# Kernel tuning notes

Measured on AMD Instinct MI355X. Metric: run time of the kernel, lower is better.

Reference implementation:

```python
import jax, jax.numpy as jnp
import numpy as np

NUM_HEADS = 16

def setup_inputs() -> dict:
    key = jax.random.key(0)
    k_x, k_wq, k_bq, k_wo, k_bo = jax.random.split(key, 5)
    B, S, D = 4, 2048, 1024
    x = jax.random.normal(k_x, (B, S, D), dtype=jnp.float32)
    # Flax Dense default init: lecun_normal for kernel, zeros for bias; use small normals here.
    w_qkv = jax.random.normal(k_wq, (D, 3 * D), dtype=jnp.float32) * (D ** -0.5)
    b_qkv = jnp.zeros((3 * D,), dtype=jnp.float32)
    w_out = jax.random.normal(k_wo, (D, D), dtype=jnp.float32) * (D ** -0.5)
    b_out = jnp.zeros((D,), dtype=jnp.float32)
    return {"x": x, "w_qkv": w_qkv, "b_qkv": b_qkv, "w_out": w_out, "b_out": b_out}

def reference(x, w_qkv, b_qkv, w_out, b_out):
    B, S, D = x.shape
    H = NUM_HEADS
    hd = D // H
    scale = hd ** -0.5
    qkv = x @ w_qkv + b_qkv                                  # [B,S,3D]
    qkv = qkv.reshape(B, S, 3, H, hd)
    qkv = jnp.transpose(qkv, (2, 0, 3, 1, 4))                # [3,B,H,S,hd]
    q, k, v = qkv[0], qkv[1], qkv[2]
    attn = jnp.einsum("bhqd,bhkd->bhqk", q, k) * scale       # [B,H,S,S]
    attn = jax.nn.softmax(attn, axis=-1)
    out = jnp.einsum("bhqk,bhkd->bhqd", attn, v)             # [B,H,S,hd]
    out = jnp.transpose(out, (0, 2, 1, 3)).reshape(B, S, D)
    return out @ w_out + b_out
```

## Files before the change

kernel.cpp:

```cpp
#include <hip/hip_runtime.h>
#include <cstdint>
#include <cstddef>

#define B_    4
#define S_    2048
#define D_    1024
#define H_    16
#define HD_   64
#define M_    8192
#define NQKV  3072

typedef __bf16 bf16;
typedef __bf16 bf16x4 __attribute__((ext_vector_type(4)));
typedef __bf16 bf16x8 __attribute__((ext_vector_type(8)));
typedef float  f32x2  __attribute__((ext_vector_type(2)));
typedef float  f32x4  __attribute__((ext_vector_type(4)));
typedef float  f32x16 __attribute__((ext_vector_type(16)));
typedef unsigned short u16x4 __attribute__((ext_vector_type(4)));
typedef uint32_t u32x2 __attribute__((ext_vector_type(2)));
typedef uint32_t u32x4 __attribute__((ext_vector_type(4)));

__device__ __forceinline__ void gl2lds16(const void* g, void* l) {
  __builtin_amdgcn_global_load_lds(
      (__attribute__((address_space(1))) void*)(uintptr_t)g,
      (__attribute__((address_space(3))) void*)l, 16, 0, 0);
}

__device__ __forceinline__ uint32_t pkbf16(float a, float b) {
  union { bf16 h[2]; uint32_t u; } z;
  z.h[0] = (bf16)a; z.h[1] = (bf16)b;
  return z.u;
}

__global__ __launch_bounds__(256) void cast_f32_bf16(const float* __restrict__ in,
                                                     bf16* __restrict__ out, int n4) {
  int i = blockIdx.x * 256 + threadIdx.x;
  if (i >= n4) return;
  float4 v = ((const float4*)in)[i];
  bf16x4 o;
  o[0] = (bf16)v.x; o[1] = (bf16)v.y; o[2] = (bf16)v.z; o[3] = (bf16)v.w;
  ((bf16x4*)out)[i] = o;
}

__global__ __launch_bounds__(256) void transpose_cast(const float* __restrict__ in,
                                                      bf16* __restrict__ out, int R, int C) {
  __shared__ float tile[32][33];
  int bx = blockIdx.x * 32, by = blockIdx.y * 32;
  int tx = threadIdx.x, ty = threadIdx.y;
#pragma unroll
  for (int i = 0; i < 32; i += 8)
    tile[ty + i][tx] = in[(size_t)(by + ty + i) * C + bx + tx];
  __syncthreads();
#pragma unroll
  for (int i = 0; i < 32; i += 8)
    out[(size_t)(bx + ty + i) * R + by + tx] = (bf16)tile[tx][ty + i];
}

template <bool OUT_BF16>
__global__ __launch_bounds__(256) void gemm_bt(const bf16* __restrict__ A,
                                               const bf16* __restrict__ Bt,
                                               const float* __restrict__ bias,
                                               void* __restrict__ Cptr,
                                               int M, int N, int K) {
  __shared__ __align__(16) bf16 As[128 * 64];
  __shared__ __align__(16) bf16 Bs[128 * 64];
  const int tid  = threadIdx.x;
  const int lane = tid & 63, w = tid >> 6;
  const int lo   = lane & 15, quad = lane >> 4;
  const int xcd = blockIdx.x & 7, g = blockIdx.x >> 3;
  const int mi  = g & 7,          n = g >> 3;
  const int bm  = (xcd * 8 + mi) * 128, bn = n * 128;
  const int wm = (w >> 1) * 64,    wn = (w & 1) * 64;

  f32x4 acc[4][4];
  const f32x4 zero = {0.f, 0.f, 0.f, 0.f};
#pragma unroll
  for (int i = 0; i < 4; ++i)
#pragma unroll
    for (int j = 0; j < 4; ++j) acc[i][j] = zero;

  for (int k0 = 0; k0 < K; k0 += 64) {
#pragma unroll
    for (int c = 0; c < 4; ++c) {
      int seg = c * 4 + w;
      int idx = seg * 512 + lane * 8;
      int row = idx >> 6, col = idx & 63;
      gl2lds16(A  + (size_t)(bm + row) * K + k0 + col, As + seg * 512);
      gl2lds16(Bt + (size_t)(bn + row) * K + k0 + col, Bs + seg * 512);
    }
    __syncthreads();
#pragma unroll
    for (int ks = 0; ks < 2; ++ks) {
      bf16x8 av[4], bv[4];
#pragma unroll
      for (int i = 0; i < 4; ++i)
        av[i] = *(const bf16x8*)&As[(wm + i * 16 + lo) * 64 + ks * 32 + quad * 8];
#pragma unroll
      for (int j = 0; j < 4; ++j)
        bv[j] = *(const bf16x8*)&Bs[(wn + j * 16 + lo) * 64 + ks * 32 + quad * 8];
#pragma unroll
      for (int i = 0; i < 4; ++i)
#pragma unroll
        for (int j = 0; j < 4; ++j)
          acc[i][j] = __builtin_amdgcn_mfma_f32_16x16x32_bf16(av[i], bv[j], acc[i][j], 0, 0, 0);
    }
    __syncthreads();
  }
#pragma unroll
  for (int j = 0; j < 4; ++j) {
    int cg = bn + wn + j * 16 + lo;
    float bsv = bias[cg];
#pragma unroll
    for (int i = 0; i < 4; ++i) {
      int rg = bm + wm + i * 16 + quad * 4;
#pragma unroll
      for (int r = 0; r < 4; ++r) {
        float v = acc[i][j][r] + bsv;
        if (OUT_BF16) ((bf16*)Cptr)[(size_t)(rg + r) * N + cg] = (bf16)v;
        else          ((float*)Cptr)[(size_t)(rg + r) * N + cg] = v;
      }
    }
  }
}

__global__ __launch_bounds__(256, 2) void gemm_bt_wide(const bf16* __restrict__ A,
                                                       const bf16* __restrict__ Bt,
                                                       const float* __restrict__ bias,
                                                       bf16* __restrict__ Cptr,
                                                       int M, int N, int K) {
  __shared__ __align__(16) bf16 As[128 * 64];
  __shared__ __align__(16) bf16 Bs[256 * 64];
  const int tid  = threadIdx.x;
  const int lane = tid & 63, w = tid >> 6;
  const int lo   = lane & 15, quad = lane >> 4;
  const int xcd = blockIdx.x & 7, g = blockIdx.x >> 3;
  const int mi  = g & 7,          n = g >> 3;
  const int bm  = (xcd * 8 + mi) * 128, bn = n * 256;
  const int wm = (w >> 1) * 64,    wn = (w & 1) * 128;

  f32x4 acc[4][8];
  const f32x4 zero = {0.f, 0.f, 0.f, 0.f};
#pragma unroll
  for (int i = 0; i < 4; ++i)
#pragma unroll
    for (int j = 0; j < 8; ++j) acc[i][j] = zero;

  for (int k0 = 0; k0 < K; k0 += 64) {
#pragma unroll
    for (int c = 0; c < 4; ++c) {
      int seg = c * 4 + w;
      int idx = seg * 512 + lane * 8;
      int row = idx >> 6, col = idx & 63;
      gl2lds16(A + (size_t)(bm + row) * K + k0 + col, As + seg * 512);
    }
#pragma unroll
    for (int c = 0; c < 8; ++c) {
      int seg = c * 4 + w;
      int idx = seg * 512 + lane * 8;
      int row = idx >> 6, col = idx & 63;
      gl2lds16(Bt + (size_t)(bn + row) * K + k0 + col, Bs + seg * 512);
    }
    __syncthreads();
#pragma unroll
    for (int ks = 0; ks < 2; ++ks) {
      bf16x8 av[4], bv[8];
#pragma unroll
      for (int i = 0; i < 4; ++i)
        av[i] = *(const bf16x8*)&As[(wm + i * 16 + lo) * 64 + ks * 32 + quad * 8];
#pragma unroll
      for (int j = 0; j < 8; ++j)
        bv[j] = *(const bf16x8*)&Bs[(wn + j * 16 + lo) * 64 + ks * 32 + quad * 8];
#pragma unroll
      for (int i = 0; i < 4; ++i)
#pragma unroll
        for (int j = 0; j < 8; ++j)
          acc[i][j] = __builtin_amdgcn_mfma_f32_16x16x32_bf16(av[i], bv[j], acc[i][j], 0, 0, 0);
    }
    __syncthreads();
  }
#pragma unroll
  for (int j = 0; j < 8; ++j) {
    int cg = bn + wn + j * 16 + lo;
    float bsv = bias[cg];
#pragma unroll
    for (int i = 0; i < 4; ++i) {
      int rg = bm + wm + i * 16 + quad * 4;
#pragma unroll
      for (int r = 0; r < 4; ++r)
        Cptr[(size_t)(rg + r) * N + cg] = (bf16)(acc[i][j][r] + bsv);
    }
  }
}

__global__ __launch_bounds__(256, 2) void flash_attn(const bf16* __restrict__ qkv,
                                                     bf16* __restrict__ out) {
  __shared__ __align__(16) bf16 smem[16384];
  bf16* const Ksm = smem;
  bf16* const Vsm = smem + 8192;

  const int tid  = threadIdx.x;
  const int lane = tid & 63, wq = tid >> 6;
  const int l31  = lane & 31;
  const int e    = lane >> 5;
  const int hi8  = e * 8, hi4 = e * 4;

  const int bid = blockIdx.x;
  const int qb  = bid >> 6;
  const int bh  = bid & 63;
  const int h   = bh & 15;
  const int b   = bh >> 4;
  const int q0  = qb * 256;
  const size_t rowb = (size_t)b * S_;
  const bf16* qbase = qkv + rowb * NQKV + h * HD_;
  const bf16* kbase = qbase + D_;
  const bf16* vbase = qbase + 2 * D_;

  bf16x8 qfA[4], qfB[4];
  {
    const bf16* qrow0 = qbase + (size_t)(q0 + wq * 64 + l31) * NQKV;
    const bf16* qrow1 = qrow0 + (size_t)32 * NQKV;
#pragma unroll
    for (int c = 0; c < 4; ++c) {
      qfA[c] = *(const bf16x8*)(qrow0 + c * 16 + hi8);
      qfB[c] = *(const bf16x8*)(qrow1 + c * 16 + hi8);
    }
  }

  int kq_off[2];
#pragma unroll
  for (int it = 0; it < 2; ++it) {
    int ci = it * 256 + tid;
    int s  = ci >> 3;
    int x  = (ci & 7) ^ (s & 7);
    kq_off[it] = s * NQKV + x * 8;
  }
  int vs_d[2], vs_s[2], vs_off[2];
#pragma unroll
  for (int u = 0; u < 2; ++u) {
    int idx = u * 256 + tid;
    int d0 = (idx & 31) * 2;
    int s0 = (idx >> 5) * 4;
    vs_d[u] = d0;
    vs_s[u] = s0;
    vs_off[u] = (((s0 >> 3) ^ ((d0 >> 1) & 7)) * 8) + (s0 & 7);
  }

  uint32_t vreg[2][4];

#pragma unroll
  for (int it = 0; it < 2; ++it)
    gl2lds16(kbase + kq_off[it], Ksm + (it * 256 + wq * 64) * 8);
#pragma unroll
  for (int u = 0; u < 2; ++u)
#pragma unroll
    for (int j = 0; j < 4; ++j)
      vreg[u][j] = *(const uint32_t*)(vbase + (size_t)(vs_s[u] + j) * NQKV + vs_d[u]);

  const f32x16 zero16 = {0.f,0.f,0.f,0.f,0.f,0.f,0.f,0.f,0.f,0.f,0.f,0.f,0.f,0.f,0.f,0.f};
  f32x16 oacc[2][2];
  oacc[0][0] = zero16; oacc[0][1] = zero16;
  oacc[1][0] = zero16; oacc[1][1] = zero16;
  f32x2 psA = {0.f, 0.f}, psB = {0.f, 0.f};
  const float c2 = 0.125f * 1.44269504088896341f;

  for (int kt = 0; kt < 32; ++kt) {
    const int buf = kt & 1;
#pragma unroll
    for (int u = 0; u < 2; ++u) {
      int d0 = vs_d[u];
      uint32_t lo0 = __builtin_amdgcn_perm(vreg[u][1], vreg[u][0], 0x05040100u);
      uint32_t lo1 = __builtin_amdgcn_perm(vreg[u][3], vreg[u][2], 0x05040100u);
      uint32_t hi0 = __builtin_amdgcn_perm(vreg[u][1], vreg[u][0], 0x07060302u);
      uint32_t hi1 = __builtin_amdgcn_perm(vreg[u][3], vreg[u][2], 0x07060302u);
      u32x2 lov = {lo0, lo1}, hiv = {hi0, hi1};
      *(u32x2*)&Vsm[buf * 4096 + (d0 + 0) * 64 + vs_off[u]] = lov;
      *(u32x2*)&Vsm[buf * 4096 + (d0 + 1) * 64 + vs_off[u]] = hiv;
    }
    __syncthreads();

    {
      int ktn = (kt + 1 < 32) ? kt + 1 : 31;
      const bf16* kb = kbase + (size_t)ktn * 64 * NQKV;
#pragma unroll
      for (int it = 0; it < 2; ++it)
        gl2lds16(kb + kq_off[it], Ksm + (buf ^ 1) * 4096 + (it * 256 + wq * 64) * 8);
    }
    {
      int ktn = (kt + 1 < 32) ? kt + 1 : 31;
      const bf16* vb = vbase + (size_t)ktn * 64 * NQKV;
#pragma unroll
      for (int u = 0; u < 2; ++u)
#pragma unroll
        for (int j = 0; j < 4; ++j)
          vreg[u][j] = *(const uint32_t*)(vb + (size_t)(vs_s[u] + j) * NQKV + vs_d[u]);
    }

#pragma unroll
    for (int kk = 0; kk < 2; ++kk) {
      f32x16 sA = zero16, sB = zero16;
      int srow = kk * 32 + l31;
      int swz  = (srow & 7) * 8;
#pragma unroll
      for (int c = 0; c < 4; ++c) {
        bf16x8 kf = *(const bf16x8*)&Ksm[buf * 4096 + srow * 64 + ((c * 16 + hi8) ^ swz)];
        sA = __builtin_amdgcn_mfma_f32_32x32x16_bf16(kf, qfA[c], sA, 0, 0, 0);
        sB = __builtin_amdgcn_mfma_f32_32x32x16_bf16(kf, qfB[c], sB, 0, 0, 0);
      }

      uint32_t Q8a[8], Q8b[8];
#pragma unroll
      for (int i = 0; i < 8; ++i) {
        f32x2 sva, svb;
        sva[0] = sA[2 * i]; sva[1] = sA[2 * i + 1];
        svb[0] = sB[2 * i]; svb[1] = sB[2 * i + 1];
        f32x2 ta = sva * c2 - 16.0f;
        f32x2 tb = svb * c2 - 16.0f;
        float a0 = __builtin_amdgcn_exp2f(ta[0]);
        float a1 = __builtin_amdgcn_exp2f(ta[1]);
        float b0 = __builtin_amdgcn_exp2f(tb[0]);
        float b1 = __builtin_amdgcn_exp2f(tb[1]);
        psA += (f32x2){a0, a1};
        psB += (f32x2){b0, b1};
        Q8a[i] = pkbf16(a0, a1);
        Q8b[i] = pkbf16(b0, b1);
      }

#pragma unroll
      for (int mh = 0; mh < 2; ++mh) {
        const int m = kk * 2 + mh, bq = mh * 4;
        u32x4 pda, pdb;
#if __has_builtin(__builtin_amdgcn_permlane32_swap)
        u32x2 wa0 = __builtin_amdgcn_permlane32_swap(Q8a[bq],     Q8a[bq + 2], false, false);
        u32x2 wa1 = __builtin_amdgcn_permlane32_swap(Q8a[bq + 1], Q8a[bq + 3], false, false);
        pda[0] = wa0[0]; pda[1] = wa1[0]; pda[2] = wa0[1]; pda[3] = wa1[1];
        u32x2 wb0 = __builtin_amdgcn_permlane32_swap(Q8b[bq],     Q8b[bq + 2], false, false);
        u32x2 wb1 = __builtin_amdgcn_permlane32_swap(Q8b[bq + 1], Q8b[bq + 3], false, false);
        pdb[0] = wb0[0]; pdb[1] = wb1[0]; pdb[2] = wb0[1]; pdb[3] = wb1[1];
#else
        {
          uint32_t s0 = e ? Q8a[bq]     : Q8a[bq + 2];
          uint32_t s1 = e ? Q8a[bq + 1] : Q8a[bq + 3];
          uint32_t r0 = __shfl_xor(s0, 32);
          uint32_t r1 = __shfl_xor(s1, 32);
          pda[0] = e ? r0 : Q8a[bq];
          pda[1] = e ? r1 : Q8a[bq + 1];
          pda[2] = e ? Q8a[bq + 2] : r0;
          pda[3] = e ? Q8a[bq + 3] : r1;
        }
        {
          uint32_t s0 = e ? Q8b[bq]     : Q8b[bq + 2];
          uint32_t s1 = e ? Q8b[bq + 1] : Q8b[bq + 3];
          uint32_t r0 = __shfl_xor(s0, 32);
          uint32_t r1 = __shfl_xor(s1, 32);
          pdb[0] = e ? r0 : Q8b[bq];
          pdb[1] = e ? r1 : Q8b[bq + 1];
          pdb[2] = e ? Q8b[bq + 2] : r0;
          pdb[3] = e ? Q8b[bq + 3] : r1;
        }
#endif
        bf16x8 pfa = __builtin_bit_cast(bf16x8, pda);
        bf16x8 pfb = __builtin_bit_cast(bf16x8, pdb);
#pragma unroll
        for (int dt = 0; dt < 2; ++dt) {
          int drow = dt * 32 + l31;
          int swv  = (drow >> 1) & 7;
          bf16x8 vf = *(const bf16x8*)&Vsm[buf * 4096 + drow * 64 + (((m * 2 + e) ^ swv) * 8)];
          oacc[dt][0] = __builtin_amdgcn_mfma_f32_32x32x16_bf16(vf, pfa, oacc[dt][0], 0, 0, 0);
          oacc[dt][1] = __builtin_amdgcn_mfma_f32_32x32x16_bf16(vf, pfb, oacc[dt][1], 0, 0, 0);
        }
      }
    }
  }

  float lsumA = psA[0] + psA[1];
  float lsumB = psB[0] + psB[1];
  lsumA += __shfl_xor(lsumA, 32);
  lsumB += __shfl_xor(lsumB, 32);

  __syncthreads();
  bf16* Os = smem;
  {
    float invA = 1.f / lsumA;
    float invB = 1.f / lsumB;
#pragma unroll
    for (int qs = 0; qs < 2; ++qs) {
      float inv = qs ? invB : invA;
      int ql = wq * 64 + qs * 32 + l31;
      int swO = (ql >> 1) & 7;
#pragma unroll
      for (int dt = 0; dt < 2; ++dt) {
#pragma unroll
        for (int g = 0; g < 4; ++g) {
          bf16x4 ov;
#pragma unroll
          for (int jj = 0; jj < 4; ++jj)
            ov[jj] = (bf16)(oacc[dt][qs][g * 4 + jj] * inv);
          *(bf16x4*)&Os[ql * 64 + (((dt * 4 + g) ^ swO) * 8) + hi4] = ov;
        }
      }
    }
  }
  __syncthreads();
#pragma unroll
  for (int it = 0; it < 8; ++it) {
    int idx = it * 256 + tid;
    int row = idx >> 3, c8 = idx & 7;
    bf16x8 t = *(const bf16x8*)&Os[row * 64 + ((c8 ^ ((row >> 1) & 7)) * 8)];
    *(bf16x8*)&out[(rowb + q0 + row) * D_ + h * HD_ + c8 * 8] = t;
  }
}

extern "C" void kernel_launch(void* const* d_in, const int* in_sizes, int n_in,
                              void* d_out, int out_size, void* d_ws, size_t ws_size,
                              hipStream_t stream) {
  const float* x     = (const float*)d_in[0];
  const float* w_qkv = (const float*)d_in[1];
  const float* b_qkv = (const float*)d_in[2];
  const float* w_out = (const float*)d_in[3];
  const float* b_out = (const float*)d_in[4];
  float* out = (float*)d_out;

  char* ws = (char*)d_ws;
  bf16* xb    = (bf16*)(ws);
  bf16* wqkvT = (bf16*)(ws + (size_t)16777216);
  bf16* woutT = (bf16*)(ws + (size_t)23068672);
  bf16* qkvb  = (bf16*)(ws + (size_t)25165824);
  bf16* attnb = (bf16*)(ws + (size_t)75497472);

  cast_f32_bf16<<<(M_ * D_ / 4 + 255) / 256, 256, 0, stream>>>(x, xb, M_ * D_ / 4);
  transpose_cast<<<dim3(NQKV / 32, D_ / 32), dim3(32, 8), 0, stream>>>(w_qkv, wqkvT, D_, NQKV);
  transpose_cast<<<dim3(D_ / 32, D_ / 32), dim3(32, 8), 0, stream>>>(w_out, woutT, D_, D_);

  gemm_bt_wide<<<(M_ / 128) * (NQKV / 256), 256, 0, stream>>>(
      xb, wqkvT, b_qkv, qkvb, M_, NQKV, D_);

  flash_attn<<<B_ * H_ * (S_ / 256), 256, 0, stream>>>(qkvb, attnb);

  gemm_bt<false><<<(M_ / 128) * (D_ / 128), 256, 0, stream>>>(
      attnb, woutT, b_out, (void*)out, M_, D_, D_);
}
```

Measured before the change: 283.2 us.

## Deepen K/V prefetch pipeline and raise wave priority around MFMA blocks

The attention loop is restructured so that the K tile's async global-to-LDS copy for the next step and the V register loads two steps ahead are issued before compute. The V transpose-write into the other LDS buffer moves after compute, and each step ends with one explicit waitcnt plus barrier. This removes the mid-iteration barrier and hides global-load latency behind the MFMA work. s_setprio is also raised around the MFMA groups so waves doing matrix work get issue priority. The cost is a second set of V staging registers, which adds register pressure, and a hand-written vmcnt that depends on the exact order in which loads are issued.

```diff
diff --git a/kernel.cpp b/kernel.cpp
--- a/kernel.cpp
+++ b/kernel.cpp
@@ -245,16 +245,7 @@
     vs_off[u] = (((s0 >> 3) ^ ((d0 >> 1) & 7)) * 8) + (s0 & 7);
   }
 
-  uint32_t vreg[2][4];
-
-#pragma unroll
-  for (int it = 0; it < 2; ++it)
-    gl2lds16(kbase + kq_off[it], Ksm + (it * 256 + wq * 64) * 8);
-#pragma unroll
-  for (int u = 0; u < 2; ++u)
-#pragma unroll
-    for (int j = 0; j < 4; ++j)
-      vreg[u][j] = *(const uint32_t*)(vbase + (size_t)(vs_s[u] + j) * NQKV + vs_d[u]);
+  uint32_t vE[2][4], vO[2][4];
 
   const f32x16 zero16 = {0.f,0.f,0.f,0.f,0.f,0.f,0.f,0.f,0.f,0.f,0.f,0.f,0.f,0.f,0.f,0.f};
   f32x16 oacc[2][2];
@@ -263,49 +254,48 @@
   f32x2 psA = {0.f, 0.f}, psB = {0.f, 0.f};
   const float c2 = 0.125f * 1.44269504088896341f;
 
-  for (int kt = 0; kt < 32; ++kt) {
-    const int buf = kt & 1;
-#pragma unroll
-    for (int u = 0; u < 2; ++u) {
-      int d0 = vs_d[u];
-      uint32_t lo0 = __builtin_amdgcn_perm(vreg[u][1], vreg[u][0], 0x05040100u);
-      uint32_t lo1 = __builtin_amdgcn_perm(vreg[u][3], vreg[u][2], 0x05040100u);
-      uint32_t hi0 = __builtin_amdgcn_perm(vreg[u][1], vreg[u][0], 0x07060302u);
-      uint32_t hi1 = __builtin_amdgcn_perm(vreg[u][3], vreg[u][2], 0x07060302u);
-      u32x2 lov = {lo0, lo1}, hiv = {hi0, hi1};
-      *(u32x2*)&Vsm[buf * 4096 + (d0 + 0) * 64 + vs_off[u]] = lov;
-      *(u32x2*)&Vsm[buf * 4096 + (d0 + 1) * 64 + vs_off[u]] = hiv;
-    }
-    __syncthreads();
-
-    {
-      int ktn = (kt + 1 < 32) ? kt + 1 : 31;
-      const bf16* kb = kbase + (size_t)ktn * 64 * NQKV;
-#pragma unroll
-      for (int it = 0; it < 2; ++it)
-        gl2lds16(kb + kq_off[it], Ksm + (buf ^ 1) * 4096 + (it * 256 + wq * 64) * 8);
-    }
-    {
-      int ktn = (kt + 1 < 32) ? kt + 1 : 31;
-      const bf16* vb = vbase + (size_t)ktn * 64 * NQKV;
-#pragma unroll
-      for (int u = 0; u < 2; ++u)
-#pragma unroll
-        for (int j = 0; j < 4; ++j)
-          vreg[u][j] = *(const uint32_t*)(vb + (size_t)(vs_s[u] + j) * NQKV + vs_d[u]);
-    }
-
+#define KDMA(KT, PB) {                                                      \
+    const bf16* kb_ = kbase + (size_t)(KT) * 64 * NQKV;                     \
+    _Pragma("unroll")                                                       \
+    for (int it = 0; it < 2; ++it)                                          \
+      gl2lds16(kb_ + kq_off[it], Ksm + (PB) * 4096 + (it * 256 + wq * 64) * 8); \
+  }
+#define VLOAD(KT, VR) {                                                     \
+    const bf16* vb_ = vbase + (size_t)(KT) * 64 * NQKV;                     \
+    _Pragma("unroll")                                                       \
+    for (int u = 0; u < 2; ++u)                                             \
+      _Pragma("unroll")                                                     \
+      for (int j = 0; j < 4; ++j)                                           \
+        VR[u][j] = *(const uint32_t*)(vb_ + (size_t)(vs_s[u] + j) * NQKV + vs_d[u]); \
+  }
+#define VWRITE(VR, PB) {                                                    \
+    _Pragma("unroll")                                                       \
+    for (int u = 0; u < 2; ++u) {                                           \
+      int d0_ = vs_d[u];                                                    \
+      uint32_t lo0 = __builtin_amdgcn_perm(VR[u][1], VR[u][0], 0x05040100u);\
+      uint32_t lo1 = __builtin_amdgcn_perm(VR[u][3], VR[u][2], 0x05040100u);\
+      uint32_t hi0 = __builtin_amdgcn_perm(VR[u][1], VR[u][0], 0x07060302u);\
+      uint32_t hi1 = __builtin_amdgcn_perm(VR[u][3], VR[u][2], 0x07060302u);\
+      u32x2 lov = {lo0, lo1}, hiv = {hi0, hi1};                             \
+      *(u32x2*)&Vsm[(PB) * 4096 + (d0_ + 0) * 64 + vs_off[u]] = lov;        \
+      *(u32x2*)&Vsm[(PB) * 4096 + (d0_ + 1) * 64 + vs_off[u]] = hiv;        \
+    }                                                                       \
+  }
+
+  auto compute = [&](int P) __attribute__((always_inline)) {
 #pragma unroll
     for (int kk = 0; kk < 2; ++kk) {
       f32x16 sA = zero16, sB = zero16;
       int srow = kk * 32 + l31;
       int swz  = (srow & 7) * 8;
+      __builtin_amdgcn_s_setprio(1);
 #pragma unroll
       for (int c = 0; c < 4; ++c) {
-        bf16x8 kf = *(const bf16x8*)&Ksm[buf * 4096 + srow * 64 + ((c * 16 + hi8) ^ swz)];
+        bf16x8 kf = *(const bf16x8*)&Ksm[P * 4096 + srow * 64 + ((c * 16 + hi8) ^ swz)];
         sA = __builtin_amdgcn_mfma_f32_32x32x16_bf16(kf, qfA[c], sA, 0, 0, 0);
         sB = __builtin_amdgcn_mfma_f32_32x32x16_bf16(kf, qfB[c], sB, 0, 0, 0);
       }
+      __builtin_amdgcn_s_setprio(0);
 
       uint32_t Q8a[8], Q8b[8];
 #pragma unroll
@@ -360,17 +350,46 @@
 #endif
         bf16x8 pfa = __builtin_bit_cast(bf16x8, pda);
         bf16x8 pfb = __builtin_bit_cast(bf16x8, pdb);
+        __builtin_amdgcn_s_setprio(1);
 #pragma unroll
         for (int dt = 0; dt < 2; ++dt) {
           int drow = dt * 32 + l31;
           int swv  = (drow >> 1) & 7;
-          bf16x8 vf = *(const bf16x8*)&Vsm[buf * 4096 + drow * 64 + (((m * 2 + e) ^ swv) * 8)];
+          bf16x8 vf = *(const bf16x8*)&Vsm[P * 4096 + drow * 64 + (((m * 2 + e) ^ swv) * 8)];
           oacc[dt][0] = __builtin_amdgcn_mfma_f32_32x32x16_bf16(vf, pfa, oacc[dt][0], 0, 0, 0);
           oacc[dt][1] = __builtin_amdgcn_mfma_f32_32x32x16_bf16(vf, pfb, oacc[dt][1], 0, 0, 0);
         }
+        __builtin_amdgcn_s_setprio(0);
       }
     }
-  }
+  };
+
+#define BODY(KT, P, VWR, VLD) {                                             \
+    int kn1 = (KT) + 1 < 32 ? (KT) + 1 : 31;                                \
+    int kn2 = (KT) + 2 < 32 ? (KT) + 2 : 31;                                \
+    KDMA(kn1, (P) ^ 1);                           \
+    VLOAD(kn2, VLD);               \
+    compute(P);                                                             \
+    VWRITE(VWR, (P) ^ 1);                  \
+    asm volatile("s_waitcnt vmcnt(8) lgkmcnt(0)" ::: "memory");             \
+    __builtin_amdgcn_s_barrier();                                           \
+  }
+
+  KDMA(0, 0);
+  VLOAD(0, vE);
+  VLOAD(1, vO);
+  VWRITE(vE, 0);
+  asm volatile("s_waitcnt vmcnt(8) lgkmcnt(0)" ::: "memory");
+  __builtin_amdgcn_s_barrier();
+
+  for (int t = 0; t < 16; ++t) {
+    BODY(2 * t,     0, vO, vE);
+    BODY(2 * t + 1, 1, vE, vO);
+  }
+#undef BODY
+#undef VWRITE
+#undef VLOAD
+#undef KDMA
 
   float lsumA = psA[0] + psA[1];
   float lsumB = psB[0] + psB[1];
```

Result: no change. 286.2 us (+1.1%).

## Split flash attention KV range across two wave groups and merge partial outputs

Applied to the files above, without the earlier changes.

Doubles the attention block to 512 threads: two groups of four waves each process half of the key/value sequence for the same 256 queries, with separate LDS buffers. Partial row sums and output accumulators are combined through LDS at the end before normalising and writing. It also raises wave priority around the MFMA sections with s_setprio. This is meant to shorten each block's serial KV loop and raise waves per CU, at the cost of double the LDS per block and an extra reduction pass. Skipping the running max remains safe here because the fixed exp offset is reused unchanged.

```diff
diff --git a/kernel.cpp b/kernel.cpp
--- a/kernel.cpp
+++ b/kernel.cpp
@@ -192,17 +192,18 @@
   }
 }
 
-__global__ __launch_bounds__(256, 2) void flash_attn(const bf16* __restrict__ qkv,
+__global__ __launch_bounds__(512, 4) void flash_attn(const bf16* __restrict__ qkv,
                                                      bf16* __restrict__ out) {
-  __shared__ __align__(16) bf16 smem[16384];
-  bf16* const Ksm = smem;
-  bf16* const Vsm = smem + 8192;
+  __shared__ __align__(16) bf16 smem[32768];
 
   const int tid  = threadIdx.x;
-  const int lane = tid & 63, wq = tid >> 6;
+  const int lane = tid & 63;
+  const int wq   = (tid >> 6) & 3;
+  const int grp  = tid >> 8;
+  const int t8   = tid & 255;
   const int l31  = lane & 31;
   const int e    = lane >> 5;
-  const int hi8  = e * 8, hi4 = e * 4;
+  const int hi8  = e * 8;
 
   const int bid = blockIdx.x;
   const int qb  = bid >> 6;
@@ -212,8 +213,11 @@
   const int q0  = qb * 256;
   const size_t rowb = (size_t)b * S_;
   const bf16* qbase = qkv + rowb * NQKV + h * HD_;
-  const bf16* kbase = qbase + D_;
-  const bf16* vbase = qbase + 2 * D_;
+  const bf16* kbase = qbase + D_     + (size_t)(grp * 16) * 64 * NQKV;
+  const bf16* vbase = qbase + 2 * D_ + (size_t)(grp * 16) * 64 * NQKV;
+
+  bf16* const Ksg = smem + grp * 16384;
+  bf16* const Vsg = Ksg + 8192;
 
   bf16x8 qfA[4], qfB[4];
   {
@@ -229,7 +233,7 @@
   int kq_off[2];
 #pragma unroll
   for (int it = 0; it < 2; ++it) {
-    int ci = it * 256 + tid;
+    int ci = it * 256 + t8;
     int s  = ci >> 3;
     int x  = (ci & 7) ^ (s & 7);
     kq_off[it] = s * NQKV + x * 8;
@@ -237,7 +241,7 @@
   int vs_d[2], vs_s[2], vs_off[2];
 #pragma unroll
   for (int u = 0; u < 2; ++u) {
-    int idx = u * 256 + tid;
+    int idx = u * 256 + t8;
     int d0 = (idx & 31) * 2;
     int s0 = (idx >> 5) * 4;
     vs_d[u] = d0;
@@ -249,7 +253,7 @@
 
 #pragma unroll
   for (int it = 0; it < 2; ++it)
-    gl2lds16(kbase + kq_off[it], Ksm + (it * 256 + wq * 64) * 8);
+    gl2lds16(kbase + kq_off[it], Ksg + (it * 256 + wq * 64) * 8);
 #pragma unroll
   for (int u = 0; u < 2; ++u)
 #pragma unroll
@@ -263,7 +267,7 @@
   f32x2 psA = {0.f, 0.f}, psB = {0.f, 0.f};
   const float c2 = 0.125f * 1.44269504088896341f;
 
-  for (int kt = 0; kt < 32; ++kt) {
+  for (int kt = 0; kt < 16; ++kt) {
     const int buf = kt & 1;
 #pragma unroll
     for (int u = 0; u < 2; ++u) {
@@ -273,20 +277,20 @@
       uint32_t hi0 = __builtin_amdgcn_perm(vreg[u][1], vreg[u][0], 0x07060302u);
       uint32_t hi1 = __builtin_amdgcn_perm(vreg[u][3], vreg[u][2], 0x07060302u);
       u32x2 lov = {lo0, lo1}, hiv = {hi0, hi1};
-      *(u32x2*)&Vsm[buf * 4096 + (d0 + 0) * 64 + vs_off[u]] = lov;
-      *(u32x2*)&Vsm[buf * 4096 + (d0 + 1) * 64 + vs_off[u]] = hiv;
+      *(u32x2*)&Vsg[buf * 4096 + (d0 + 0) * 64 + vs_off[u]] = lov;
+      *(u32x2*)&Vsg[buf * 4096 + (d0 + 1) * 64 + vs_off[u]] = hiv;
     }
     __syncthreads();
 
     {
-      int ktn = (kt + 1 < 32) ? kt + 1 : 31;
+      int ktn = (kt + 1 < 16) ? kt + 1 : 15;
       const bf16* kb = kbase + (size_t)ktn * 64 * NQKV;
 #pragma unroll
       for (int it = 0; it < 2; ++it)
-        gl2lds16(kb + kq_off[it], Ksm + (buf ^ 1) * 4096 + (it * 256 + wq * 64) * 8);
+        gl2lds16(kb + kq_off[it], Ksg + (buf ^ 1) * 4096 + (it * 256 + wq * 64) * 8);
     }
     {
-      int ktn = (kt + 1 < 32) ? kt + 1 : 31;
+      int ktn = (kt + 1 < 16) ? kt + 1 : 15;
       const bf16* vb = vbase + (size_t)ktn * 64 * NQKV;
 #pragma unroll
       for (int u = 0; u < 2; ++u)
@@ -300,12 +304,14 @@
       f32x16 sA = zero16, sB = zero16;
       int srow = kk * 32 + l31;
       int swz  = (srow & 7) * 8;
+      __builtin_amdgcn_s_setprio(1);
 #pragma unroll
       for (int c = 0; c < 4; ++c) {
-        bf16x8 kf = *(const bf16x8*)&Ksm[buf * 4096 + srow * 64 + ((c * 16 + hi8) ^ swz)];
+        bf16x8 kf = *(const bf16x8*)&Ksg[buf * 4096 + srow * 64 + ((c * 16 + hi8) ^ swz)];
         sA = __builtin_amdgcn_mfma_f32_32x32x16_bf16(kf, qfA[c], sA, 0, 0, 0);
         sB = __builtin_amdgcn_mfma_f32_32x32x16_bf16(kf, qfB[c], sB, 0, 0, 0);
       }
+      __builtin_amdgcn_s_setprio(0);
 
       uint32_t Q8a[8], Q8b[8];
 #pragma unroll
@@ -360,14 +366,16 @@
 #endif
         bf16x8 pfa = __builtin_bit_cast(bf16x8, pda);
         bf16x8 pfb = __builtin_bit_cast(bf16x8, pdb);
+        __builtin_amdgcn_s_setprio(1);
 #pragma unroll
         for (int dt = 0; dt < 2; ++dt) {
           int drow = dt * 32 + l31;
           int swv  = (drow >> 1) & 7;
-          bf16x8 vf = *(const bf16x8*)&Vsm[buf * 4096 + drow * 64 + (((m * 2 + e) ^ swv) * 8)];
+          bf16x8 vf = *(const bf16x8*)&Vsg[buf * 4096 + drow * 64 + (((m * 2 + e) ^ swv) * 8)];
           oacc[dt][0] = __builtin_amdgcn_mfma_f32_32x32x16_bf16(vf, pfa, oacc[dt][0], 0, 0, 0);
           oacc[dt][1] = __builtin_amdgcn_mfma_f32_32x32x16_bf16(vf, pfb, oacc[dt][1], 0, 0, 0);
         }
+        __builtin_amdgcn_s_setprio(0);
       }
     }
   }
@@ -377,36 +385,82 @@
   lsumA += __shfl_xor(lsumA, 32);
   lsumB += __shfl_xor(lsumB, 32);
 
-  __syncthreads();
-  bf16* Os = smem;
-  {
-    float invA = 1.f / lsumA;
-    float invB = 1.f / lsumB;
-#pragma unroll
-    for (int qs = 0; qs < 2; ++qs) {
+  float* const S4 = (float*)smem;
+
+  __syncthreads();
+  if (e == 0) {
+    S4[grp * 256 + wq * 64 + l31]      = lsumA;
+    S4[grp * 256 + wq * 64 + 32 + l31] = lsumB;
+  }
+  __syncthreads();
+  float invA = 0.f, invB = 0.f;
+  if (grp == 1) {
+    invA = 1.f / (S4[wq * 64 + l31]      + lsumA);
+    invB = 1.f / (S4[wq * 64 + 32 + l31] + lsumB);
+  }
+  __syncthreads();
+
+  if (grp == 0) {
+#pragma unroll
+    for (int dt = 0; dt < 2; ++dt)
+#pragma unroll
+      for (int qs = 0; qs < 2; ++qs)
+#pragma unroll
+        for (int hi = 0; hi < 4; ++hi) {
+          int l = qs * 32 + l31;
+          int c = (dt * 8 + 2 * hi + e) ^ (l & 15);
+          f32x4 v4;
+          v4[0] = oacc[dt][qs][hi * 4 + 0];
+          v4[1] = oacc[dt][qs][hi * 4 + 1];
+          v4[2] = oacc[dt][qs][hi * 4 + 2];
+          v4[3] = oacc[dt][qs][hi * 4 + 3];
+          *(f32x4*)&S4[wq * 4096 + l * 64 + c * 4] = v4;
+        }
+  }
+  __syncthreads();
+
+  if (grp == 1) {
+#pragma unroll
+    for (int qs = 1; qs >= 0; --qs) {
+      int l = qs * 32 + l31;
       float inv = qs ? invB : invA;
-      int ql = wq * 64 + qs * 32 + l31;
-      int swO = (ql >> 1) & 7;
-#pragma unroll
-      for (int dt = 0; dt < 2; ++dt) {
-#pragma unroll
-        for (int g = 0; g < 4; ++g) {
+      f32x4 po[8];
+#pragma unroll
+      for (int dt = 0; dt < 2; ++dt)
+#pragma unroll
+        for (int hi = 0; hi < 4; ++hi) {
+          int c = (dt * 8 + 2 * hi + e) ^ (l & 15);
+          po[dt * 4 + hi] = *(const f32x4*)&S4[wq * 4096 + l * 64 + c * 4];
+        }
+#pragma unroll
+      for (int dt = 0; dt < 2; ++dt)
+#pragma unroll
+        for (int hi = 0; hi < 4; ++hi) {
           bf16x4 ov;
 #pragma unroll
-          for (int jj = 0; jj < 4; ++jj)
-            ov[jj] = (bf16)(oacc[dt][qs][g * 4 + jj] * inv);
-          *(bf16x4*)&Os[ql * 64 + (((dt * 4 + g) ^ swO) * 8) + hi4] = ov;
-        }
-      }
-    }
-  }
-  __syncthreads();
-#pragma unroll
-  for (int it = 0; it < 8; ++it) {
-    int idx = it * 256 + tid;
-    int row = idx >> 3, c8 = idx & 7;
-    bf16x8 t = *(const bf16x8*)&Os[row * 64 + ((c8 ^ ((row >> 1) & 7)) * 8)];
-    *(bf16x8*)&out[(rowb + q0 + row) * D_ + h * HD_ + c8 * 8] = t;
+          for (int j = 0; j < 4; ++j)
+            ov[j] = (bf16)((po[dt * 4 + hi][j] + oacc[dt][qs][hi * 4 + j]) * inv);
+          int hc = (dt * 8 + 2 * hi + e) ^ (l & 15);
+          *(bf16x4*)&smem[wq * 8192 + 4096 + l * 64 + hc * 4] = ov;
+        }
+    }
+  }
+  __syncthreads();
+
+#pragma unroll
+  for (int it = 0; it < 4; ++it) {
+    int idx = it * 512 + tid;
+    int q = idx >> 3, k8 = idx & 7;
+    int ws_ = q >> 6, l = q & 63;
+    int base = ws_ * 8192 + 4096 + l * 64;
+    int h0 = (2 * k8)     ^ (l & 15);
+    int h1 = (2 * k8 + 1) ^ (l & 15);
+    bf16x4 a = *(const bf16x4*)&smem[base + h0 * 4];
+    bf16x4 bb = *(const bf16x4*)&smem[base + h1 * 4];
+    bf16x8 t;
+    t[0] = a[0]; t[1] = a[1]; t[2] = a[2]; t[3] = a[3];
+    t[4] = bb[0]; t[5] = bb[1]; t[6] = bb[2]; t[7] = bb[3];
+    *(bf16x8*)&out[(rowb + q0 + q) * D_ + h * HD_ + k8 * 8] = t;
   }
 }
 
@@ -434,7 +488,7 @@
   gemm_bt_wide<<<(M_ / 128) * (NQKV / 256), 256, 0, stream>>>(
       xb, wqkvT, b_qkv, qkvb, M_, NQKV, D_);
 
-  flash_attn<<<B_ * H_ * (S_ / 256), 256, 0, stream>>>(qkvb, attnb);
+  flash_attn<<<B_ * H_ * (S_ / 256), 512, 0, stream>>>(qkvb, attnb);
 
   gemm_bt<false><<<(M_ / 128) * (D_ / 128), 256, 0, stream>>>(
       attnb, woutT, b_out, (void*)out, M_, D_, D_);
```

New measurement: 493.3 us. 1.74x slower.

## Split attention KV range across two blocks and combine partial results

Applied to the files above, without the earlier changes.

Each attention block now covers half the key/value sequence, which doubles the grid from 512 to 1024 blocks for better CU fill on the large GPU. Unnormalized fp32 partial outputs and row sums go to workspace, and a new combine kernel sums them, normalizes and writes bf16. This works because the fixed-offset exp (no running max) makes the partials directly additive. MFMA sections are also wrapped in s_setprio raises. The cost is extra global traffic for the fp32 partials, one more launch, and dependence on workspace size, with a fallback to the unsplit path.

```diff
diff --git a/kernel.cpp b/kernel.cpp
--- a/kernel.cpp
+++ b/kernel.cpp
@@ -16,7 +16,6 @@
 typedef float  f32x2  __attribute__((ext_vector_type(2)));
 typedef float  f32x4  __attribute__((ext_vector_type(4)));
 typedef float  f32x16 __attribute__((ext_vector_type(16)));
-typedef unsigned short u16x4 __attribute__((ext_vector_type(4)));
 typedef uint32_t u32x2 __attribute__((ext_vector_type(2)));
 typedef uint32_t u32x4 __attribute__((ext_vector_type(4)));
 
@@ -192,8 +191,11 @@
   }
 }
 
-__global__ __launch_bounds__(256, 2) void flash_attn(const bf16* __restrict__ qkv,
-                                                     bf16* __restrict__ out) {
+template <int SPLIT>
+__global__ __launch_bounds__(256, 2) void flash_attn_k(const bf16* __restrict__ qkv,
+                                                       bf16* __restrict__ out,
+                                                       float* __restrict__ opart,
+                                                       float* __restrict__ lpart) {
   __shared__ __align__(16) bf16 smem[16384];
   bf16* const Ksm = smem;
   bf16* const Vsm = smem + 8192;
@@ -205,15 +207,18 @@
   const int hi8  = e * 8, hi4 = e * 4;
 
   const int bid = blockIdx.x;
-  const int qb  = bid >> 6;
-  const int bh  = bid & 63;
+  const int ob  = SPLIT ? (bid >> 1) : bid;
+  const int grp = SPLIT ? (bid & 1) : 0;
+  const int NT  = SPLIT ? 16 : 32;
+  const int qb  = ob >> 6;
+  const int bh  = ob & 63;
   const int h   = bh & 15;
   const int b   = bh >> 4;
   const int q0  = qb * 256;
   const size_t rowb = (size_t)b * S_;
   const bf16* qbase = qkv + rowb * NQKV + h * HD_;
-  const bf16* kbase = qbase + D_;
-  const bf16* vbase = qbase + 2 * D_;
+  const bf16* kbase = qbase + D_     + (size_t)(grp * 16) * 64 * NQKV;
+  const bf16* vbase = qbase + 2 * D_ + (size_t)(grp * 16) * 64 * NQKV;
 
   bf16x8 qfA[4], qfB[4];
   {
@@ -263,7 +268,7 @@
   f32x2 psA = {0.f, 0.f}, psB = {0.f, 0.f};
   const float c2 = 0.125f * 1.44269504088896341f;
 
-  for (int kt = 0; kt < 32; ++kt) {
+  for (int kt = 0; kt < NT; ++kt) {
     const int buf = kt & 1;
 #pragma unroll
     for (int u = 0; u < 2; ++u) {
@@ -279,14 +284,14 @@
     __syncthreads();
 
     {
-      int ktn = (kt + 1 < 32) ? kt + 1 : 31;
+      int ktn = (kt + 1 < NT) ? kt + 1 : NT - 1;
       const bf16* kb = kbase + (size_t)ktn * 64 * NQKV;
 #pragma unroll
       for (int it = 0; it < 2; ++it)
         gl2lds16(kb + kq_off[it], Ksm + (buf ^ 1) * 4096 + (it * 256 + wq * 64) * 8);
     }
     {
-      int ktn = (kt + 1 < 32) ? kt + 1 : 31;
+      int ktn = (kt + 1 < NT) ? kt + 1 : NT - 1;
       const bf16* vb = vbase + (size_t)ktn * 64 * NQKV;
 #pragma unroll
       for (int u = 0; u < 2; ++u)
@@ -300,12 +305,14 @@
       f32x16 sA = zero16, sB = zero16;
       int srow = kk * 32 + l31;
       int swz  = (srow & 7) * 8;
+      __builtin_amdgcn_s_setprio(1);
 #pragma unroll
       for (int c = 0; c < 4; ++c) {
         bf16x8 kf = *(const bf16x8*)&Ksm[buf * 4096 + srow * 64 + ((c * 16 + hi8) ^ swz)];
         sA = __builtin_amdgcn_mfma_f32_32x32x16_bf16(kf, qfA[c], sA, 0, 0, 0);
         sB = __builtin_amdgcn_mfma_f32_32x32x16_bf16(kf, qfB[c], sB, 0, 0, 0);
       }
+      __builtin_amdgcn_s_setprio(0);
 
       uint32_t Q8a[8], Q8b[8];
 #pragma unroll
@@ -360,6 +367,7 @@
 #endif
         bf16x8 pfa = __builtin_bit_cast(bf16x8, pda);
         bf16x8 pfb = __builtin_bit_cast(bf16x8, pdb);
+        __builtin_amdgcn_s_setprio(1);
 #pragma unroll
         for (int dt = 0; dt < 2; ++dt) {
           int drow = dt * 32 + l31;
@@ -368,6 +376,7 @@
           oacc[dt][0] = __builtin_amdgcn_mfma_f32_32x32x16_bf16(vf, pfa, oacc[dt][0], 0, 0, 0);
           oacc[dt][1] = __builtin_amdgcn_mfma_f32_32x32x16_bf16(vf, pfb, oacc[dt][1], 0, 0, 0);
         }
+        __builtin_amdgcn_s_setprio(0);
       }
     }
   }
@@ -377,36 +386,94 @@
   lsumA += __shfl_xor(lsumA, 32);
   lsumB += __shfl_xor(lsumB, 32);
 
-  __syncthreads();
-  bf16* Os = smem;
-  {
-    float invA = 1.f / lsumA;
-    float invB = 1.f / lsumB;
+  if (SPLIT) {
+    float* obase = opart + (size_t)bid * (256 * 64);
+    if (e == 0) {
+      lpart[bid * 256 + wq * 64 + l31]      = lsumA;
+      lpart[bid * 256 + wq * 64 + 32 + l31] = lsumB;
+    }
 #pragma unroll
     for (int qs = 0; qs < 2; ++qs) {
-      float inv = qs ? invB : invA;
-      int ql = wq * 64 + qs * 32 + l31;
-      int swO = (ql >> 1) & 7;
-#pragma unroll
-      for (int dt = 0; dt < 2; ++dt) {
+      float* oq = obase + (size_t)(wq * 64 + qs * 32 + l31) * 64;
+#pragma unroll
+      for (int dt = 0; dt < 2; ++dt)
 #pragma unroll
         for (int g = 0; g < 4; ++g) {
-          bf16x4 ov;
-#pragma unroll
-          for (int jj = 0; jj < 4; ++jj)
-            ov[jj] = (bf16)(oacc[dt][qs][g * 4 + jj] * inv);
-          *(bf16x4*)&Os[ql * 64 + (((dt * 4 + g) ^ swO) * 8) + hi4] = ov;
+          f32x4 v4;
+          v4[0] = oacc[dt][qs][g * 4 + 0];
+          v4[1] = oacc[dt][qs][g * 4 + 1];
+          v4[2] = oacc[dt][qs][g * 4 + 2];
+          v4[3] = oacc[dt][qs][g * 4 + 3];
+          *(f32x4*)&oq[dt * 32 + g * 8 + e * 4] = v4;
+        }
+    }
+  } else {
+    __syncthreads();
+    bf16* Os = smem;
+    {
+      float invA = 1.f / lsumA;
+      float invB = 1.f / lsumB;
+#pragma unroll
+      for (int qs = 0; qs < 2; ++qs) {
+        float inv = qs ? invB : invA;
+        int ql = wq * 64 + qs * 32 + l31;
+        int swO = (ql >> 1) & 7;
+#pragma unroll
+        for (int dt = 0; dt < 2; ++dt) {
+#pragma unroll
+          for (int g = 0; g < 4; ++g) {
+            bf16x4 ov;
+#pragma unroll
+            for (int jj = 0; jj < 4; ++jj)
+              ov[jj] = (bf16)(oacc[dt][qs][g * 4 + jj] * inv);
+            *(bf16x4*)&Os[ql * 64 + (((dt * 4 + g) ^ swO) * 8) + hi4] = ov;
+          }
         }
       }
     }
-  }
-  __syncthreads();
-#pragma unroll
-  for (int it = 0; it < 8; ++it) {
-    int idx = it * 256 + tid;
-    int row = idx >> 3, c8 = idx & 7;
-    bf16x8 t = *(const bf16x8*)&Os[row * 64 + ((c8 ^ ((row >> 1) & 7)) * 8)];
-    *(bf16x8*)&out[(rowb + q0 + row) * D_ + h * HD_ + c8 * 8] = t;
+    __syncthreads();
+#pragma unroll
+    for (int it = 0; it < 8; ++it) {
+      int idx = it * 256 + tid;
+      int row = idx >> 3, c8 = idx & 7;
+      bf16x8 t = *(const bf16x8*)&Os[row * 64 + ((c8 ^ ((row >> 1) & 7)) * 8)];
+      *(bf16x8*)&out[(rowb + q0 + row) * D_ + h * HD_ + c8 * 8] = t;
+    }
+  }
+}
+
+__global__ __launch_bounds__(256) void combine_parts(const float* __restrict__ opart,
+                                                     const float* __restrict__ lpart,
+                                                     bf16* __restrict__ out) {
+  const int ob = blockIdx.x;
+  const int qb = ob >> 6, bh = ob & 63;
+  const int h  = bh & 15, b = bh >> 4;
+  const int q0 = qb * 256;
+  const size_t rowb = (size_t)b * S_;
+  const float* o0 = opart + (size_t)(2 * ob) * (256 * 64);
+  const float* o1 = o0 + 256 * 64;
+  const float* l0 = lpart + (size_t)(2 * ob) * 256;
+  const float* l1 = l0 + 256;
+  const int tid = threadIdx.x;
+#pragma unroll
+  for (int rep = 0; rep < 4; ++rep) {
+    int flat = rep * 4096 + tid * 16;
+    int q = flat >> 6, d0 = flat & 63;
+    float inv = 1.f / (l0[q] + l1[q]);
+    bf16* dst = out + (rowb + q0 + q) * D_ + h * HD_ + d0;
+#pragma unroll
+    for (int half = 0; half < 2; ++half) {
+      bf16x8 t;
+#pragma unroll
+      for (int c = 0; c < 2; ++c) {
+        f32x4 x = *(const f32x4*)&o0[(size_t)q * 64 + d0 + half * 8 + c * 4];
+        f32x4 y = *(const f32x4*)&o1[(size_t)q * 64 + d0 + half * 8 + c * 4];
+#pragma unroll
+        for (int j = 0; j < 4; ++j)
+          t[c * 4 + j] = (bf16)((x[j] + y[j]) * inv);
+      }
+      *(bf16x8*)&dst[half * 8] = t;
+    }
   }
 }
 
@@ -421,11 +488,14 @@
   float* out = (float*)d_out;
 
   char* ws = (char*)d_ws;
-  bf16* xb    = (bf16*)(ws);
-  bf16* wqkvT = (bf16*)(ws + (size_t)16777216);
-  bf16* woutT = (bf16*)(ws + (size_t)23068672);
-  bf16* qkvb  = (bf16*)(ws + (size_t)25165824);
-  bf16* attnb = (bf16*)(ws + (size_t)75497472);
+  bf16*  xb    = (bf16*)(ws);
+  bf16*  attnb = (bf16*)(ws);
+  bf16*  wqkvT = (bf16*)(ws + (size_t)16777216);
+  bf16*  woutT = (bf16*)(ws + (size_t)23068672);
+  bf16*  qkvb  = (bf16*)(ws + (size_t)25165824);
+  float* opart = (float*)(ws + (size_t)75497472);
+  float* lpart = (float*)(ws + (size_t)142606336);
+  const size_t WS_NEED_SPLIT = 143654912;
 
   cast_f32_bf16<<<(M_ * D_ / 4 + 255) / 256, 256, 0, stream>>>(x, xb, M_ * D_ / 4);
   transpose_cast<<<dim3(NQKV / 32, D_ / 32), dim3(32, 8), 0, stream>>>(w_qkv, wqkvT, D_, NQKV);
@@ -434,7 +504,12 @@
   gemm_bt_wide<<<(M_ / 128) * (NQKV / 256), 256, 0, stream>>>(
       xb, wqkvT, b_qkv, qkvb, M_, NQKV, D_);
 
-  flash_attn<<<B_ * H_ * (S_ / 256), 256, 0, stream>>>(qkvb, attnb);
+  if (ws_size >= WS_NEED_SPLIT) {
+    flash_attn_k<1><<<B_ * H_ * (S_ / 256) * 2, 256, 0, stream>>>(qkvb, attnb, opart, lpart);
+    combine_parts<<<B_ * H_ * (S_ / 256), 256, 0, stream>>>(opart, lpart, attnb);
+  } else {
+    flash_attn_k<0><<<B_ * H_ * (S_ / 256), 256, 0, stream>>>(qkvb, attnb, nullptr, nullptr);
+  }
 
   gemm_bt<false><<<(M_ / 128) * (D_ / 128), 256, 0, stream>>>(
       attnb, woutT, b_out, (void*)out, M_, D_, D_);
```

Measured after the change: 307.2 us. 8.5% more time.
